# Kernel optimization log

Hardware: AMD Instinct MI355X
Metric: run time of the kernel (lower is better)

The kernel has to match this reference:

```python
import jax, jax.numpy as jnp
import numpy as np

N_NODES = 50000

def setup_inputs() -> dict:
    key = jax.random.key(0)
    k1, k2, k3 = jax.random.split(key, 3)
    d = 128
    E = 800000
    x = jax.random.normal(k1, (N_NODES, d), dtype=jnp.float32)
    edge_index = jax.random.randint(k2, (2, E), 0, N_NODES, dtype=jnp.int64)
    # Glorot-ish init for GCN weight
    W = jax.random.normal(k3, (d, d), dtype=jnp.float32) * (1.0 / np.sqrt(d))
    b = jnp.zeros((d,), dtype=jnp.float32)
    t = jnp.zeros((1,), dtype=jnp.float32)
    return {"t": t, "x": x, "edge_index": edge_index, "W": W, "b": b}


def reference(t, x, edge_index, W, b):
    # GCNConv (PyG defaults): add self-loops, symmetric normalization,
    # out = D^{-1/2} (A+I) D^{-1/2} (x W) + b, followed by tanh activation.
    n = x.shape[0]
    self_loops = jnp.arange(n, dtype=edge_index.dtype)
    row = jnp.concatenate([edge_index[0], self_loops])  # source
    col = jnp.concatenate([edge_index[1], self_loops])  # target

    ones = jnp.ones_like(col, dtype=x.dtype)
    deg = jax.ops.segment_sum(ones, col, num_segments=n)  # in-degree incl. self-loop
    deg_inv_sqrt = jnp.where(deg > 0, jax.lax.rsqrt(deg), 0.0)
    norm = deg_inv_sqrt[row] * deg_inv_sqrt[col]  # [E+N]

    h = x @ W  # [N, d] linear transform first (GCNConv order)
    msg = h[row] * norm[:, None]  # gather + scale, [E+N, d]
    out = jax.ops.segment_sum(msg, col, num_segments=n)  # scatter-add to targets
    out = out + b
    return jnp.tanh(out)
```

## Files before the change

### kernel.cpp

```cpp
#include <hip/hip_runtime.h>
#include <math.h>


#define D 128
#define CAP 64

typedef unsigned int uint;
typedef unsigned short ushort;

__device__ __forceinline__ uint bf16pair(float a, float b) {
    uint ua = __float_as_uint(a);
    ua = (ua + 0x7FFFu + ((ua >> 16) & 1u)) >> 16;
    uint ub = __float_as_uint(b);
    ub = (ub + 0x7FFFu + ((ub >> 16) & 1u)) >> 16;
    return ua | (ub << 16);
}
__device__ __forceinline__ float bf_lo(uint u) { return __uint_as_float(u << 16); }
__device__ __forceinline__ float bf_hi(uint u) { return __uint_as_float(u & 0xFFFF0000u); }

__global__ void k_zero(int* __restrict__ deg, int n) {
    int i = blockIdx.x * 256 + threadIdx.x;
    if (i < n) deg[i] = 0;
}

__global__ void k_build(const int* __restrict__ rows, const int* __restrict__ cols,
                        int* __restrict__ deg, int* __restrict__ csr, int E) {
    int e = blockIdx.x * 256 + threadIdx.x;
    if (e < E) {
        int c = cols[e];
        int p = atomicAdd(&deg[c], 1);
        if (p < CAP) csr[c * CAP + p] = rows[e];
    }
}

__global__ __launch_bounds__(256) void k_gemm(const float* __restrict__ x,
                                              const float* __restrict__ W,
                                              const int* __restrict__ deg,
                                              ushort* __restrict__ hs, int n) {
    __shared__ float Wl[32][132];
    __shared__ float Xl[64][33];
    const int tid = threadIdx.x;
    const int tx = tid & 15;
    const int ty = tid >> 4;
    const int m0 = blockIdx.x * 64;

    float acc[4][8];
#pragma unroll
    for (int i = 0; i < 4; ++i)
#pragma unroll
        for (int j = 0; j < 8; ++j) acc[i][j] = 0.f;

    for (int k0 = 0; k0 < 128; k0 += 32) {
        {
            const int kk = tid >> 3;
            const int cb = (tid & 7) * 16;
#pragma unroll
            for (int j = 0; j < 4; ++j) {
                float4 w = *(const float4*)&W[(k0 + kk) * D + cb + j * 4];
                Wl[kk][cb + j * 4 + 0] = w.x;
                Wl[kk][cb + j * 4 + 1] = w.y;
                Wl[kk][cb + j * 4 + 2] = w.z;
                Wl[kk][cb + j * 4 + 3] = w.w;
            }
        }
        {
            const int r = tid >> 2;
            const int kb = (tid & 3) * 8;
            const int m = m0 + r;
#pragma unroll
            for (int j = 0; j < 2; ++j) {
                float4 v = make_float4(0.f, 0.f, 0.f, 0.f);
                if (m < n) v = *(const float4*)&x[m * D + k0 + kb + j * 4];
                Xl[r][kb + j * 4 + 0] = v.x;
                Xl[r][kb + j * 4 + 1] = v.y;
                Xl[r][kb + j * 4 + 2] = v.z;
                Xl[r][kb + j * 4 + 3] = v.w;
            }
        }
        __syncthreads();

#pragma unroll
        for (int kk = 0; kk < 32; ++kk) {
            float xv[4];
#pragma unroll
            for (int i = 0; i < 4; ++i) xv[i] = Xl[ty * 4 + i][kk];
            float4 wa = *(const float4*)&Wl[kk][tx * 8];
            float4 wb = *(const float4*)&Wl[kk][tx * 8 + 4];
#pragma unroll
            for (int i = 0; i < 4; ++i) {
                acc[i][0] += xv[i] * wa.x;
                acc[i][1] += xv[i] * wa.y;
                acc[i][2] += xv[i] * wa.z;
                acc[i][3] += xv[i] * wa.w;
                acc[i][4] += xv[i] * wb.x;
                acc[i][5] += xv[i] * wb.y;
                acc[i][6] += xv[i] * wb.z;
                acc[i][7] += xv[i] * wb.w;
            }
        }
        __syncthreads();
    }

#pragma unroll
    for (int i = 0; i < 4; ++i) {
        int m = m0 + ty * 4 + i;
        if (m < n) {
            float s = rsqrtf((float)deg[m] + 1.0f);
            uint4 o;
            o.x = bf16pair(acc[i][0] * s, acc[i][1] * s);
            o.y = bf16pair(acc[i][2] * s, acc[i][3] * s);
            o.z = bf16pair(acc[i][4] * s, acc[i][5] * s);
            o.w = bf16pair(acc[i][6] * s, acc[i][7] * s);
            *(uint4*)&hs[(size_t)m * D + tx * 8] = o;
        }
    }
}

__global__ __launch_bounds__(256) void k_gather(const ushort* __restrict__ hs,
                                                const int* __restrict__ csr,
                                                const int* __restrict__ deg,
                                                const float* __restrict__ bvec,
                                                float* __restrict__ out, int n) {
    int wave = threadIdx.x >> 6;
    int lane = threadIdx.x & 63;
    int c = blockIdx.x * 4 + wave;
    if (c >= n) return;
    const uint* h2 = (const uint*)hs;

    uint u = h2[(size_t)c * 64 + lane];
    float ax = bf_lo(u), ay = bf_hi(u);

    int nd = deg[c];
    if (nd > CAP) nd = CAP;
    const int* lst = csr + (size_t)c * CAP;

    int j = 0;
    for (; j + 8 <= nd; j += 8) {
        int s0 = lst[j + 0], s1 = lst[j + 1], s2 = lst[j + 2], s3 = lst[j + 3];
        int s4 = lst[j + 4], s5 = lst[j + 5], s6 = lst[j + 6], s7 = lst[j + 7];
        uint u0 = h2[(size_t)s0 * 64 + lane];
        uint u1 = h2[(size_t)s1 * 64 + lane];
        uint u2 = h2[(size_t)s2 * 64 + lane];
        uint u3 = h2[(size_t)s3 * 64 + lane];
        uint u4 = h2[(size_t)s4 * 64 + lane];
        uint u5 = h2[(size_t)s5 * 64 + lane];
        uint u6 = h2[(size_t)s6 * 64 + lane];
        uint u7 = h2[(size_t)s7 * 64 + lane];
        ax += ((bf_lo(u0) + bf_lo(u1)) + (bf_lo(u2) + bf_lo(u3))) +
              ((bf_lo(u4) + bf_lo(u5)) + (bf_lo(u6) + bf_lo(u7)));
        ay += ((bf_hi(u0) + bf_hi(u1)) + (bf_hi(u2) + bf_hi(u3))) +
              ((bf_hi(u4) + bf_hi(u5)) + (bf_hi(u6) + bf_hi(u7)));
    }
    for (; j < nd; ++j) {
        int s = lst[j];
        uint us = h2[(size_t)s * 64 + lane];
        ax += bf_lo(us);
        ay += bf_hi(us);
    }

    float sc = rsqrtf((float)nd + 1.0f);
    float2 bb = ((const float2*)bvec)[lane];
    float2 o;
    o.x = tanhf(ax * sc + bb.x);
    o.y = tanhf(ay * sc + bb.y);
    ((float2*)out)[(size_t)c * 64 + lane] = o;
}

extern "C" void kernel_launch(void* const* d_in, const int* in_sizes, int n_in,
                              void* d_out, int out_size, void* d_ws, size_t ws_size,
                              hipStream_t stream) {
    const float* x  = (const float*)d_in[1];
    const int*   ei = (const int*)d_in[2];
    const float* W  = (const float*)d_in[3];
    const float* b  = (const float*)d_in[4];
    float* out = (float*)d_out;

    const int n = in_sizes[1] / D;
    const int E = in_sizes[2] / 2;
    const int* rows = ei;
    const int* cols = ei + E;

    char* ws = (char*)d_ws;
    int*    deg = (int*)(ws + 0x000000);
    int*    csr = (int*)(ws + 0x100000);
    ushort* hs  = (ushort*)(ws + 0xE00000);

    k_zero<<<(n + 255) / 256, 256, 0, stream>>>(deg, n);
    k_build<<<(E + 255) / 256, 256, 0, stream>>>(rows, cols, deg, csr, E);
    k_gemm<<<(n + 63) / 64, 256, 0, stream>>>(x, W, deg, hs, n);
    k_gather<<<(n + 3) / 4, 256, 0, stream>>>(hs, csr, deg, b, out, n);
}
```

Baseline: 205.7 us.

## Fuse CSR build with GEMM and move source-degree scaling into gather

```diff
diff --git a/kernel.cpp b/kernel.cpp
--- a/kernel.cpp
+++ b/kernel.cpp
@@ -18,28 +18,28 @@
 __device__ __forceinline__ float bf_lo(uint u) { return __uint_as_float(u << 16); }
 __device__ __forceinline__ float bf_hi(uint u) { return __uint_as_float(u & 0xFFFF0000u); }
 
-__global__ void k_zero(int* __restrict__ deg, int n) {
-    int i = blockIdx.x * 256 + threadIdx.x;
-    if (i < n) deg[i] = 0;
-}
-
-__global__ void k_build(const int* __restrict__ rows, const int* __restrict__ cols,
-                        int* __restrict__ deg, int* __restrict__ csr, int E) {
-    int e = blockIdx.x * 256 + threadIdx.x;
-    if (e < E) {
-        int c = cols[e];
-        int p = atomicAdd(&deg[c], 1);
-        if (p < CAP) csr[c * CAP + p] = rows[e];
-    }
-}
-
-__global__ __launch_bounds__(256) void k_gemm(const float* __restrict__ x,
-                                              const float* __restrict__ W,
-                                              const int* __restrict__ deg,
-                                              ushort* __restrict__ hs, int n) {
+__global__ __launch_bounds__(256) void k_fused(const float* __restrict__ x,
+                                               const float* __restrict__ W,
+                                               ushort* __restrict__ hs,
+                                               const int* __restrict__ rows,
+                                               const int* __restrict__ cols,
+                                               int* __restrict__ deg,
+                                               ushort* __restrict__ csr,
+                                               int n, int E, int gemmBlocks) {
     __shared__ float Wl[32][132];
     __shared__ float Xl[64][33];
     const int tid = threadIdx.x;
+
+    if (blockIdx.x >= gemmBlocks) {
+        int e = (blockIdx.x - gemmBlocks) * 256 + tid;
+        if (e < E) {
+            int c = cols[e];
+            int p = atomicAdd(&deg[c], 1);
+            if (p < CAP) csr[c * CAP + p] = (ushort)rows[e];
+        }
+        return;
+    }
+
     const int tx = tid & 15;
     const int ty = tid >> 4;
     const int m0 = blockIdx.x * 64;
@@ -105,19 +105,18 @@
     for (int i = 0; i < 4; ++i) {
         int m = m0 + ty * 4 + i;
         if (m < n) {
-            float s = rsqrtf((float)deg[m] + 1.0f);
             uint4 o;
-            o.x = bf16pair(acc[i][0] * s, acc[i][1] * s);
-            o.y = bf16pair(acc[i][2] * s, acc[i][3] * s);
-            o.z = bf16pair(acc[i][4] * s, acc[i][5] * s);
-            o.w = bf16pair(acc[i][6] * s, acc[i][7] * s);
+            o.x = bf16pair(acc[i][0], acc[i][1]);
+            o.y = bf16pair(acc[i][2], acc[i][3]);
+            o.z = bf16pair(acc[i][4], acc[i][5]);
+            o.w = bf16pair(acc[i][6], acc[i][7]);
             *(uint4*)&hs[(size_t)m * D + tx * 8] = o;
         }
     }
 }
 
 __global__ __launch_bounds__(256) void k_gather(const ushort* __restrict__ hs,
-                                                const int* __restrict__ csr,
+                                                const ushort* __restrict__ csr,
                                                 const int* __restrict__ deg,
                                                 const float* __restrict__ bvec,
                                                 float* __restrict__ out, int n) {
@@ -127,17 +126,27 @@
     if (c >= n) return;
     const uint* h2 = (const uint*)hs;
 
+    int nd = deg[c];
+    float sc = rsqrtf((float)nd + 1.0f);
+    if (nd > CAP) nd = CAP;
+
     uint u = h2[(size_t)c * 64 + lane];
-    float ax = bf_lo(u), ay = bf_hi(u);
-
-    int nd = deg[c];
-    if (nd > CAP) nd = CAP;
-    const int* lst = csr + (size_t)c * CAP;
+    float ax = bf_lo(u) * sc, ay = bf_hi(u) * sc;
+
+    const ushort* lst = csr + (size_t)c * CAP;
 
     int j = 0;
     for (; j + 8 <= nd; j += 8) {
         int s0 = lst[j + 0], s1 = lst[j + 1], s2 = lst[j + 2], s3 = lst[j + 3];
         int s4 = lst[j + 4], s5 = lst[j + 5], s6 = lst[j + 6], s7 = lst[j + 7];
+        float w0 = rsqrtf((float)deg[s0] + 1.0f);
+        float w1 = rsqrtf((float)deg[s1] + 1.0f);
+        float w2 = rsqrtf((float)deg[s2] + 1.0f);
+        float w3 = rsqrtf((float)deg[s3] + 1.0f);
+        float w4 = rsqrtf((float)deg[s4] + 1.0f);
+        float w5 = rsqrtf((float)deg[s5] + 1.0f);
+        float w6 = rsqrtf((float)deg[s6] + 1.0f);
+        float w7 = rsqrtf((float)deg[s7] + 1.0f);
         uint u0 = h2[(size_t)s0 * 64 + lane];
         uint u1 = h2[(size_t)s1 * 64 + lane];
         uint u2 = h2[(size_t)s2 * 64 + lane];
@@ -146,19 +155,23 @@
         uint u5 = h2[(size_t)s5 * 64 + lane];
         uint u6 = h2[(size_t)s6 * 64 + lane];
         uint u7 = h2[(size_t)s7 * 64 + lane];
-        ax += ((bf_lo(u0) + bf_lo(u1)) + (bf_lo(u2) + bf_lo(u3))) +
-              ((bf_lo(u4) + bf_lo(u5)) + (bf_lo(u6) + bf_lo(u7)));
-        ay += ((bf_hi(u0) + bf_hi(u1)) + (bf_hi(u2) + bf_hi(u3))) +
-              ((bf_hi(u4) + bf_hi(u5)) + (bf_hi(u6) + bf_hi(u7)));
+        ax = fmaf(bf_lo(u0), w0, ax); ay = fmaf(bf_hi(u0), w0, ay);
+        ax = fmaf(bf_lo(u1), w1, ax); ay = fmaf(bf_hi(u1), w1, ay);
+        ax = fmaf(bf_lo(u2), w2, ax); ay = fmaf(bf_hi(u2), w2, ay);
+        ax = fmaf(bf_lo(u3), w3, ax); ay = fmaf(bf_hi(u3), w3, ay);
+        ax = fmaf(bf_lo(u4), w4, ax); ay = fmaf(bf_hi(u4), w4, ay);
+        ax = fmaf(bf_lo(u5), w5, ax); ay = fmaf(bf_hi(u5), w5, ay);
+        ax = fmaf(bf_lo(u6), w6, ax); ay = fmaf(bf_hi(u6), w6, ay);
+        ax = fmaf(bf_lo(u7), w7, ax); ay = fmaf(bf_hi(u7), w7, ay);
     }
     for (; j < nd; ++j) {
         int s = lst[j];
+        float w = rsqrtf((float)deg[s] + 1.0f);
         uint us = h2[(size_t)s * 64 + lane];
-        ax += bf_lo(us);
-        ay += bf_hi(us);
-    }
-
-    float sc = rsqrtf((float)nd + 1.0f);
+        ax = fmaf(bf_lo(us), w, ax);
+        ay = fmaf(bf_hi(us), w, ay);
+    }
+
     float2 bb = ((const float2*)bvec)[lane];
     float2 o;
     o.x = tanhf(ax * sc + bb.x);
@@ -182,11 +195,14 @@
 
     char* ws = (char*)d_ws;
     int*    deg = (int*)(ws + 0x000000);
-    int*    csr = (int*)(ws + 0x100000);
-    ushort* hs  = (ushort*)(ws + 0xE00000);
-
-    k_zero<<<(n + 255) / 256, 256, 0, stream>>>(deg, n);
-    k_build<<<(E + 255) / 256, 256, 0, stream>>>(rows, cols, deg, csr, E);
-    k_gemm<<<(n + 63) / 64, 256, 0, stream>>>(x, W, deg, hs, n);
+    ushort* csr = (ushort*)(ws + 0x100000);
+    ushort* hs  = (ushort*)(ws + 0x800000);
+
+    const int gemmBlocks  = (n + 63) / 64;
+    const int buildBlocks = (E + 255) / 256;
+
+    hipMemsetAsync(deg, 0, (size_t)n * sizeof(int), stream);
+    k_fused<<<gemmBlocks + buildBlocks, 256, 0, stream>>>(x, W, hs, rows, cols,
+                                                          deg, csr, n, E, gemmBlocks);
     k_gather<<<(n + 3) / 4, 256, 0, stream>>>(hs, csr, deg, b, out, n);
 }
```

Result: faster. 201.4 us (-2.1%).
